# Optimization experiments

Measured on AMD Instinct MI355X. Metric: run time of the kernel, lower is better.

The kernel has to match this reference:

```python
import jax, jax.numpy as jnp
import numpy as np
import math

N, E, D, H, EH, DEPTH = 50000, 800000, 128, 128, 16, 3
RATIO = 0.5
BN_SCALE = 1.0 / math.sqrt(1.0 + 1e-5)  # eval-mode BatchNorm1d: running mean 0, var 1
NEG_SLOPE = 0.01  # leaky_relu default


def setup_inputs() -> dict:
    key = jax.random.key(0)
    ks = jax.random.split(key, 16)
    s = lambda k, shape: jax.random.normal(k, shape, dtype=jnp.float32) * 0.05
    return {
        "x": jax.random.normal(ks[0], (N, D), dtype=jnp.float32),
        "edge_index": jax.random.randint(ks[1], (2, E), 0, N, dtype=jnp.int32),
        "edge_attr": jax.random.uniform(ks[2], (E, EH), dtype=jnp.float32),
        "We_w": s(ks[3], (EH, 1)), "We_b": s(ks[4], (1,)),
        "Wdown": s(ks[5], (DEPTH + 1, H, H)), "bdown": s(ks[6], (DEPTH + 1, H)),
        "Wpool": s(ks[7], (DEPTH, H)),
        "Wup": s(ks[8], (DEPTH, H, H)), "bup": s(ks[9], (DEPTH, H)),
        "gnorm": 1.0 + s(ks[10], (DEPTH + 1, H)), "bnorm": s(ks[11], (DEPTH + 1, H)),
        "Wr": s(ks[12], (D, D)), "br": s(ks[13], (D,)),
        "gr": 1.0 + s(ks[14], (D,)), "brn": s(ks[15], (D,)),
    }


def _bn(x, g, b):
    # eval-mode BatchNorm1d with running_mean=0, running_var=1
    return x * (g * BN_SCALE) + b


def _lrelu(x):
    return jnp.where(x > 0, x, NEG_SLOPE * x)


def _gcn(x, src, dst, w, W, b, fill):
    # PyG GCNConv: add self-loops (fill=1.0, improved -> 2.0), symmetric norm
    n = x.shape[0]
    h = x @ W  # [n, H]
    deg = jax.ops.segment_sum(w, dst, num_segments=n) + fill
    dinv = jax.lax.rsqrt(deg)
    coef = dinv[src] * w * dinv[dst]  # [E]
    agg = jax.ops.segment_sum(coef[:, None] * h[src], dst, num_segments=n)
    return agg + (fill / deg)[:, None] * h + b  # self-loop norm = fill/deg


def _topk_pool(x, src, dst, w, p, k):
    # PyG TopKPooling: score = tanh(x.p/||p||), keep top-k, scale kept x by score,
    # filter edges to kept nodes (masked edges kept at fixed length with weight 0)
    n = x.shape[0]
    score = jnp.tanh((x @ p) / jnp.linalg.norm(p))
    vals, perm = jax.lax.top_k(score, k)
    xp = x[perm] * vals[:, None]
    pos = jnp.full((n,), -1, dtype=jnp.int32).at[perm].set(jnp.arange(k, dtype=jnp.int32))
    ns, nd = pos[src], pos[dst]
    valid = (ns >= 0) & (nd >= 0)
    return (xp, jnp.where(valid, ns, 0), jnp.where(valid, nd, 0),
            jnp.where(valid, w, 0.0), perm)


def reference(x, edge_index, edge_attr, We_w, We_b, Wdown, bdown, Wpool, Wup, bup,
              gnorm, bnorm, Wr, br, gr, brn):
    src, dst = edge_index[0], edge_index[1]
    # edge embedding + min/max normalization
    ew = edge_attr @ We_w[:, 0] + We_b[0]  # [E]
    ew = ew - jnp.min(ew)
    ew = ew / (jnp.max(ew) + 1e-7)
    h = _bn(x, gnorm[0], bnorm[0])
    h = _lrelu(_gcn(h, src, dst, ew, Wdown[0], bdown[0], 1.0))
    xs, es, perms = [h], [(src, dst, ew)], []
    for i in range(DEPTH):
        k = int(math.ceil(RATIO * h.shape[0]))
        h, src, dst, ew, perm = _topk_pool(h, src, dst, ew, Wpool[i], k)
        h = _bn(h, gnorm[i + 1], bnorm[i + 1])
        h = _gcn(h, src, dst, ew, Wdown[i + 1], bdown[i + 1], 1.0)
        if i < DEPTH - 1:
            h = _lrelu(h)
            xs.append(h)
            es.append((src, dst, ew))
        perms.append(perm)
    for i in range(DEPTH):
        j = DEPTH - 1 - i
        res = xs[j]
        src, dst, ew = es[j]
        up = jnp.zeros_like(res).at[perms[j]].set(h)  # scatter unpool
        h = _gcn(res + up, src, dst, ew, Wup[i], bup[i], 2.0)  # improved=True -> fill 2
        if i < DEPTH - 1:
            h = _lrelu(h)
    g = jnp.sum(h, axis=0, keepdims=True)  # global_add_pool, single graph
    g = g @ Wr + br
    return _bn(g, gr, brn)
```

## Files before the change

kernel.cpp:

```cpp
#include <hip/hip_runtime.h>
#include <math.h>

#define N0   50000
#define E0   800000
#define HD   128
#define EHD  16
#define KP1  25000
#define KP2  12500
#define KP3  6250
#define BN_SCALE 0.9999950000374997f
#define NEG_SLOPE 0.01f
#define E1C  400000
#define E2C  120000
#define E3C  40000
#define NBE  782
#define CSB  782

#define NBIN   782
#define SBCAP  448
#define OVFCAP 4096

typedef int   vi4 __attribute__((ext_vector_type(4)));
typedef float vf4 __attribute__((ext_vector_type(4)));

__device__ __forceinline__ unsigned fenc(float f) {
    unsigned u = __float_as_uint(f);
    return (u & 0x80000000u) ? ~u : (u | 0x80000000u);
}
__device__ __forceinline__ unsigned packbf2(float a, float b) {
    unsigned ua = __float_as_uint(a);
    unsigned ub = __float_as_uint(b);
    ua = (ua + 0x7FFFu + ((ua >> 16) & 1u)) >> 16;
    ub = (ub + 0x7FFFu + ((ub >> 16) & 1u)) >> 16;
    return ua | (ub << 16);
}
__device__ __forceinline__ void bf8_fma(float* acc, uint4 h, float c) {
    acc[0] += c * __uint_as_float(h.x << 16);
    acc[1] += c * __uint_as_float(h.x & 0xFFFF0000u);
    acc[2] += c * __uint_as_float(h.y << 16);
    acc[3] += c * __uint_as_float(h.y & 0xFFFF0000u);
    acc[4] += c * __uint_as_float(h.z << 16);
    acc[5] += c * __uint_as_float(h.z & 0xFFFF0000u);
    acc[6] += c * __uint_as_float(h.w << 16);
    acc[7] += c * __uint_as_float(h.w & 0xFFFF0000u);
}

__global__ void k_edge_ew(const float* __restrict__ ea, const float* __restrict__ Ww,
                          const float* __restrict__ Wb, float* __restrict__ ew,
                          float2* __restrict__ partials, int E) {
    int e = blockIdx.x * 256 + threadIdx.x;
    float mn = 3.4e38f, mx = -3.4e38f;
    if (e < E) {
        const float4* a4 = (const float4*)(ea + (size_t)e * EHD);
        float s = Wb[0];
        #pragma unroll
        for (int q = 0; q < 4; ++q) {
            float4 a = a4[q];
            s += a.x * Ww[q*4+0] + a.y * Ww[q*4+1] + a.z * Ww[q*4+2] + a.w * Ww[q*4+3];
        }
        ew[e] = s;
        mn = s; mx = s;
    }
    #pragma unroll
    for (int off = 32; off > 0; off >>= 1) {
        mn = fminf(mn, __shfl_xor(mn, off));
        mx = fmaxf(mx, __shfl_xor(mx, off));
    }
    __shared__ float smn[4], smx[4];
    int lane = threadIdx.x & 63, wid = threadIdx.x >> 6;
    if (lane == 0) { smn[wid] = mn; smx[wid] = mx; }
    __syncthreads();
    if (threadIdx.x == 0) {
        float a = fminf(fminf(smn[0], smn[1]), fminf(smn[2], smn[3]));
        float b = fmaxf(fmaxf(smx[0], smx[1]), fmaxf(smx[2], smx[3]));
        partials[blockIdx.x] = make_float2(a, b);
    }
}

__global__ void __launch_bounds__(1024)
k_reduce_mm(const float2* __restrict__ partials, int nb, float* __restrict__ mmv) {
    float mn = 3.4e38f, mx = -3.4e38f;
    for (int i = threadIdx.x; i < nb; i += 1024) {
        float2 t = partials[i];
        mn = fminf(mn, t.x); mx = fmaxf(mx, t.y);
    }
    #pragma unroll
    for (int off = 32; off > 0; off >>= 1) {
        mn = fminf(mn, __shfl_xor(mn, off));
        mx = fmaxf(mx, __shfl_xor(mx, off));
    }
    __shared__ float smn[16], smx[16];
    int lane = threadIdx.x & 63, wid = threadIdx.x >> 6;
    if (lane == 0) { smn[wid] = mn; smx[wid] = mx; }
    __syncthreads();
    if (threadIdx.x == 0) {
        for (int w = 1; w < 16; ++w) { mn = fminf(mn, smn[w]); mx = fmaxf(mx, smx[w]); }
        mmv[0] = mn; mmv[1] = mx;
    }
}

__global__ void __launch_bounds__(256)
k_ew_norm_stage(float* __restrict__ ew, const float* __restrict__ mmv,
                const int* __restrict__ src, const int* __restrict__ dst,
                int* __restrict__ cnt, int* __restrict__ subCnt,
                uint2* __restrict__ staging,
                int4* __restrict__ ovfList, int* __restrict__ ovfCnt, int E) {
    unsigned xcd;
    asm volatile("s_getreg_b32 %0, hwreg(HW_REG_XCC_ID)" : "=s"(xcd));
    int e = blockIdx.x * 256 + threadIdx.x;
    if (e >= E) return;
    float mn = mmv[0];
    float sc = 1.0f / ((mmv[1] - mn) + 1e-7f);
    float w = (ew[e] - mn) * sc;
    ew[e] = w;
    if (w == 0.0f) return;
    int d = dst[e];
    int s = src[e];
    atomicAdd(&cnt[d], 1);
    int sb = (int)xcd * NBIN + (d >> 6);
    int slot = atomicAdd(&subCnt[sb], 1);
    if (slot < SBCAP) {
        staging[(size_t)sb * SBCAP + slot] =
            make_uint2((unsigned)s | ((unsigned)(d & 63) << 16), __float_as_uint(w));
    } else {
        int o = atomicAdd(ovfCnt, 1);
        if (o < OVFCAP) ovfList[o] = make_int4(s, d, __float_as_int(w), 0);
    }
}

#define GT_ROWS 64
__global__ void __launch_bounds__(256)
k_gemm128(const float* __restrict__ A, const float* __restrict__ W,
          unsigned* __restrict__ Cb, int n,
          const float* __restrict__ gs, const float* __restrict__ gb,
          const float* __restrict__ up_h, const int* __restrict__ up_pos) {
    __shared__ float As[GT_ROWS][132];
    int tid = threadIdx.x;
    int row0 = blockIdx.x * GT_ROWS;
    int maxr = n - row0;
    {
        #pragma unroll
        for (int it = 0; it < 8; ++it) {
            int idx = it * 256 + tid;
            int r = idx >> 5, q = idx & 31;
            float4 v = make_float4(0.f, 0.f, 0.f, 0.f);
            if (r < maxr) {
                v = ((const float4*)(A + (size_t)(row0 + r) * HD))[q];
                if (up_pos) {
                    int sl = up_pos[row0 + r];
                    if (sl >= 0) {
                        float4 u = ((const float4*)(up_h + (size_t)sl * HD))[q];
                        v.x += u.x; v.y += u.y; v.z += u.z; v.w += u.w;
                    }
                }
                if (gs) {
                    float4 g4 = ((const float4*)gs)[q];
                    float4 b4 = ((const float4*)gb)[q];
                    v.x = v.x * (g4.x * BN_SCALE) + b4.x;
                    v.y = v.y * (g4.y * BN_SCALE) + b4.y;
                    v.z = v.z * (g4.z * BN_SCALE) + b4.z;
                    v.w = v.w * (g4.w * BN_SCALE) + b4.w;
                }
            }
            *(float4*)&As[r][q * 4] = v;
        }
    }
    __syncthreads();
    int cg = tid & 31;
    int rg = tid >> 5;
    float4 acc[8];
    #pragma unroll
    for (int j = 0; j < 8; ++j) acc[j] = make_float4(0.f, 0.f, 0.f, 0.f);
    const float4* W4 = (const float4*)W;
    #pragma unroll 4
    for (int k = 0; k < HD; k += 4) {
        float4 w0 = W4[(k + 0) * 32 + cg];
        float4 w1 = W4[(k + 1) * 32 + cg];
        float4 w2 = W4[(k + 2) * 32 + cg];
        float4 w3 = W4[(k + 3) * 32 + cg];
        #pragma unroll
        for (int jj = 0; jj < 4; ++jj) {
            float4 a = *(const float4*)&As[4 * rg + jj][k];
            acc[jj].x += a.x * w0.x + a.y * w1.x + a.z * w2.x + a.w * w3.x;
            acc[jj].y += a.x * w0.y + a.y * w1.y + a.z * w2.y + a.w * w3.y;
            acc[jj].z += a.x * w0.z + a.y * w1.z + a.z * w2.z + a.w * w3.z;
            acc[jj].w += a.x * w0.w + a.y * w1.w + a.z * w2.w + a.w * w3.w;
        }
        #pragma unroll
        for (int jj = 0; jj < 4; ++jj) {
            float4 a = *(const float4*)&As[32 + 4 * rg + jj][k];
            acc[4 + jj].x += a.x * w0.x + a.y * w1.x + a.z * w2.x + a.w * w3.x;
            acc[4 + jj].y += a.x * w0.y + a.y * w1.y + a.z * w2.y + a.w * w3.y;
            acc[4 + jj].z += a.x * w0.z + a.y * w1.z + a.z * w2.z + a.w * w3.z;
            acc[4 + jj].w += a.x * w0.w + a.y * w1.w + a.z * w2.w + a.w * w3.w;
        }
    }
    #pragma unroll
    for (int jj = 0; jj < 4; ++jj) {
        int r = 4 * rg + jj;
        if (r < maxr) {
            uint2 pk = make_uint2(packbf2(acc[jj].x, acc[jj].y), packbf2(acc[jj].z, acc[jj].w));
            ((uint2*)(Cb + (size_t)(row0 + r) * 64))[cg] = pk;
        }
    }
    #pragma unroll
    for (int jj = 0; jj < 4; ++jj) {
        int r = 32 + 4 * rg + jj;
        if (r < maxr) {
            uint2 pk = make_uint2(packbf2(acc[4+jj].x, acc[4+jj].y), packbf2(acc[4+jj].z, acc[4+jj].w));
            ((uint2*)(Cb + (size_t)(row0 + r) * 64))[cg] = pk;
        }
    }
}

__global__ void k_sum_scan(const int* __restrict__ cnt, int* __restrict__ bsum, int n,
                           int* __restrict__ totalOut, unsigned* __restrict__ dctr) {
    int base = blockIdx.x * 1024;
    int s = 0;
    #pragma unroll
    for (int it = 0; it < 4; ++it) {
        int i = base + it * 256 + threadIdx.x;
        if (i < n) s += cnt[i];
    }
    __shared__ int ws[4];
    __shared__ int lastFlag;
    int lane = threadIdx.x & 63, wid = threadIdx.x >> 6;
    #pragma unroll
    for (int off = 32; off > 0; off >>= 1) s += __shfl_down(s, off);
    if (lane == 0) ws[wid] = s;
    __syncthreads();
    if (threadIdx.x == 0) {
        __hip_atomic_store(&bsum[blockIdx.x], ws[0] + ws[1] + ws[2] + ws[3],
                           __ATOMIC_RELAXED, __HIP_MEMORY_SCOPE_AGENT);
        unsigned prev = __hip_atomic_fetch_add(dctr, 1u, __ATOMIC_ACQ_REL, __HIP_MEMORY_SCOPE_AGENT);
        lastFlag = (prev == gridDim.x - 1);
    }
    __syncthreads();
    if (!lastFlag) return;
    if (threadIdx.x < 64) {
        int nb = gridDim.x;
        int t = threadIdx.x;
        int v = (t < nb) ? __hip_atomic_load(&bsum[t], __ATOMIC_RELAXED, __HIP_MEMORY_SCOPE_AGENT) : 0;
        int x = v;
        #pragma unroll
        for (int off = 1; off < 64; off <<= 1) {
            int y = __shfl_up(x, off);
            if (t >= off) x += y;
        }
        if (t < nb) bsum[t] = x - v;
        if (t == nb - 1) totalOut[0] = x;
    }
    if (threadIdx.x == 0)
        __hip_atomic_store(dctr, 0u, __ATOMIC_RELAXED, __HIP_MEMORY_SCOPE_AGENT);
}

__global__ void k_chunk_scan(const int* __restrict__ cnt, const int* __restrict__ bo,
                             int* __restrict__ rowptr, int* __restrict__ cursor, int n) {
    __shared__ int wsum[4];
    __shared__ int running;
    int base = blockIdx.x * 1024;
    if (threadIdx.x == 0) running = bo[blockIdx.x];
    __syncthreads();
    int lane = threadIdx.x & 63, wid = threadIdx.x >> 6;
    #pragma unroll
    for (int it = 0; it < 4; ++it) {
        int i = base + it * 256 + threadIdx.x;
        int v = (i < n) ? cnt[i] : 0;
        int x = v;
        #pragma unroll
        for (int off = 1; off < 64; off <<= 1) {
            int y = __shfl_up(x, off);
            if (lane >= off) x += y;
        }
        if (lane == 63) wsum[wid] = x;
        __syncthreads();
        int wb = 0;
        for (int w = 0; w < wid; ++w) wb += wsum[w];
        int excl = running + wb + x - v;
        if (i < n) { rowptr[i] = excl; cursor[i] = excl; }
        __syncthreads();
        if (threadIdx.x == 0) running += wsum[0] + wsum[1] + wsum[2] + wsum[3];
        __syncthreads();
    }
}

__global__ void k_csr_fill(const int* __restrict__ src, const int* __restrict__ dst,
                           const float* __restrict__ w, int* __restrict__ cursor,
                           int2* __restrict__ csr,
                           const int* __restrict__ EinPtr, int EinImm) {
    int Ein = EinPtr ? EinPtr[0] : EinImm;
    int e = blockIdx.x * 256 + threadIdx.x;
    if (e >= Ein) return;
    float wv = w[e];
    if (wv == 0.0f) return;
    int slot = atomicAdd(&cursor[dst[e]], 1);
    csr[slot] = make_int2(src[e], __float_as_int(wv));
}

__global__ void __launch_bounds__(256)
k_binB(const int* __restrict__ rowptr, const int* __restrict__ subCnt,
       const uint2* __restrict__ staging, int2* __restrict__ csr,
       int* __restrict__ cursor, float* __restrict__ sumW, int n) {
    __shared__ int   lcur[64];
    __shared__ float lw[64];
    __shared__ int2  img[2048];
    int b = blockIdx.x;
    int v0 = b * 64;
    int v1 = min(n, v0 + 64);
    int base = rowptr[v0];
    int total = rowptr[v1] - base;
    if (threadIdx.x < 64) {
        int v = v0 + threadIdx.x;
        lcur[threadIdx.x] = (v < v1) ? rowptr[v] - base : 0;
        lw[threadIdx.x] = 0.f;
    }
    __syncthreads();
    #pragma unroll 1
    for (int x = 0; x < 8; ++x) {
        int sb = x * NBIN + b;
        int cnt = min(subCnt[sb], SBCAP);
        const uint2* st = staging + (size_t)sb * SBCAP;
        for (int i = threadIdx.x; i < cnt; i += 256) {
            uint2 en = st[i];
            int dloc = (en.x >> 16) & 63;
            float wv = __uint_as_float(en.y);
            int slot = atomicAdd(&lcur[dloc], 1);
            if (slot < 2048) img[slot] = make_int2((int)(en.x & 0xFFFFu), (int)en.y);
            atomicAdd(&lw[dloc], wv);
        }
    }
    __syncthreads();
    for (int i = threadIdx.x; i < total; i += 256)
        csr[base + i] = img[i];
    if (threadIdx.x < 64) {
        int v = v0 + threadIdx.x;
        if (v < v1) {
            cursor[v] = base + lcur[threadIdx.x];
            sumW[v]   = lw[threadIdx.x];
        }
    }
}

__global__ void k_binOvf(const int4* __restrict__ ovfList, const int* __restrict__ ovfCnt,
                         int* __restrict__ cursor, int2* __restrict__ csr,
                         float* __restrict__ sumW) {
    int cnt = min(ovfCnt[0], OVFCAP);
    for (int i = threadIdx.x; i < cnt; i += 256) {
        int4 e = ovfList[i];
        int slot = atomicAdd(&cursor[e.y], 1);
        csr[slot] = make_int2(e.x, e.z);
        atomicAdd(&sumW[e.y], __int_as_float(e.z));
    }
}

__global__ void k_deg_dinv(const int* __restrict__ rowptr, const int2* __restrict__ csr,
                           float fill, float* __restrict__ deg, float* __restrict__ dinv, int n) {
    int v = blockIdx.x * 256 + threadIdx.x;
    if (v >= n) return;
    float s = fill;
    int rs = rowptr[v], re = rowptr[v + 1];
    for (int j = rs; j < re; ++j) s += __int_as_float(csr[j].y);
    deg[v] = s;
    dinv[v] = rsqrtf(s);
}

__global__ void k_deg_dinv_d(const float* __restrict__ sumW, float fill,
                             float* __restrict__ deg, float* __restrict__ dinv, int n) {
    int v = blockIdx.x * 256 + threadIdx.x;
    if (v >= n) return;
    float s = fill + sumW[v];
    deg[v] = s;
    dinv[v] = rsqrtf(s);
}

__global__ void __launch_bounds__(256)
k_gcn_gather(const int* __restrict__ rowptr, const int2* __restrict__ csr,
             const float* __restrict__ deg, const float* __restrict__ dinv,
             const unsigned* __restrict__ hWb,
             const float* __restrict__ bias,
             float fill, int n, int lrelu, float* __restrict__ out) {
    int v = blockIdx.x * 4 + (threadIdx.x >> 6);
    int lane = threadIdx.x & 63;
    if (v >= n) return;
    int rs = rowptr[v], re = rowptr[v + 1];
    float dv = dinv[v];
    int quarter = lane >> 4;
    int qi = lane & 15;
    float acc[8];
    #pragma unroll
    for (int i = 0; i < 8; ++i) acc[i] = 0.f;
    for (int base = rs; base < re; base += 64) {
        int idx = base + lane;
        int s_r = 0; float c_r = 0.f;
        if (idx < re) {
            int2 ent = csr[idx];
            s_r = ent.x;
            c_r = dinv[s_r] * __int_as_float(ent.y) * dv;
        }
        int cnt = min(64, re - base);
        int groups = cnt >> 2;
        int t = 0;
        for (; t + 1 < groups; t += 2) {
            int j0 = 4 * t + quarter, j1 = j0 + 4;
            int   s0 = __shfl(s_r, j0); float c0 = __shfl(c_r, j0);
            int   s1 = __shfl(s_r, j1); float c1 = __shfl(c_r, j1);
            uint4 h0 = ((const uint4*)(hWb + (size_t)s0 * 64))[qi];
            uint4 h1 = ((const uint4*)(hWb + (size_t)s1 * 64))[qi];
            bf8_fma(acc, h0, c0);
            bf8_fma(acc, h1, c1);
        }
        for (; t < groups; ++t) {
            int j = 4 * t + quarter;
            int s = __shfl(s_r, j); float c = __shfl(c_r, j);
            uint4 h = ((const uint4*)(hWb + (size_t)s * 64))[qi];
            bf8_fma(acc, h, c);
        }
        int rem = cnt & 3;
        if (quarter < rem) {
            int j = groups * 4 + quarter;
            int s = __shfl(s_r, j); float c = __shfl(c_r, j);
            uint4 h = ((const uint4*)(hWb + (size_t)s * 64))[qi];
            bf8_fma(acc, h, c);
        }
    }
    #pragma unroll
    for (int i = 0; i < 8; ++i) {
        acc[i] += __shfl_xor(acc[i], 16);
        acc[i] += __shfl_xor(acc[i], 32);
    }
    if (quarter == 0) {
        uint4 hs = ((const uint4*)(hWb + (size_t)v * 64))[qi];
        float sc = fill / deg[v];
        float hv[8];
        hv[0] = __uint_as_float(hs.x << 16); hv[1] = __uint_as_float(hs.x & 0xFFFF0000u);
        hv[2] = __uint_as_float(hs.y << 16); hv[3] = __uint_as_float(hs.y & 0xFFFF0000u);
        hv[4] = __uint_as_float(hs.z << 16); hv[5] = __uint_as_float(hs.z & 0xFFFF0000u);
        hv[6] = __uint_as_float(hs.w << 16); hv[7] = __uint_as_float(hs.w & 0xFFFF0000u);
        float4 b0 = ((const float4*)bias)[2 * qi];
        float4 b1 = ((const float4*)bias)[2 * qi + 1];
        float o[8];
        o[0] = acc[0] + sc * hv[0] + b0.x;
        o[1] = acc[1] + sc * hv[1] + b0.y;
        o[2] = acc[2] + sc * hv[2] + b0.z;
        o[3] = acc[3] + sc * hv[3] + b0.w;
        o[4] = acc[4] + sc * hv[4] + b1.x;
        o[5] = acc[5] + sc * hv[5] + b1.y;
        o[6] = acc[6] + sc * hv[6] + b1.z;
        o[7] = acc[7] + sc * hv[7] + b1.w;
        if (lrelu) {
            #pragma unroll
            for (int i = 0; i < 8; ++i) o[i] = (o[i] > 0.f) ? o[i] : NEG_SLOPE * o[i];
        }
        float4* orow = (float4*)(out + (size_t)v * HD);
        orow[2 * qi]     = make_float4(o[0], o[1], o[2], o[3]);
        orow[2 * qi + 1] = make_float4(o[4], o[5], o[6], o[7]);
    }
}

__global__ void k_score(const float* __restrict__ x, const float* __restrict__ p,
                        float* __restrict__ score, int n, int* __restrict__ selws) {
    for (int i = blockIdx.x * 256 + threadIdx.x; i < 5120; i += gridDim.x * 256) selws[i] = 0;
    int lane = threadIdx.x & 63;
    float pv0 = p[lane], pv1 = p[lane + 64];
    float ps = pv0 * pv0 + pv1 * pv1;
    #pragma unroll
    for (int off = 32; off > 0; off >>= 1) ps += __shfl_xor(ps, off);
    float rnorm = 1.0f / sqrtf(ps);
    int node = blockIdx.x * 4 + (threadIdx.x >> 6);
    if (node >= n) return;
    const float* row = x + (size_t)node * HD;
    float s = row[lane] * pv0 + row[lane + 64] * pv1;
    #pragma unroll
    for (int off = 32; off > 0; off >>= 1) s += __shfl_xor(s, off);
    if (lane == 0) score[node] = tanhf(s * rnorm);
}

__global__ void __launch_bounds__(256)
k_histpick(const float* __restrict__ score, int n, int pass,
           unsigned* __restrict__ prefix, int* __restrict__ hist,
           int kImm, const int* __restrict__ remIn, int* __restrict__ remOut,
           unsigned* __restrict__ doneCtr) {
    __shared__ int lh[2048];
    int nbins = (pass == 2) ? 1024 : 2048;
    for (int i = threadIdx.x; i < nbins; i += 256) lh[i] = 0;
    __syncthreads();
    unsigned pfx = (pass != 0) ? prefix[0] : 0u;
    int stride = gridDim.x * 256;
    for (int i = blockIdx.x * 256 + threadIdx.x; i < n; i += stride) {
        unsigned u = fenc(score[i]);
        int bin; bool ok;
        if (pass == 0)      { bin = u >> 21;            ok = true; }
        else if (pass == 1) { bin = (u >> 10) & 2047;   ok = ((u >> 21) == (pfx >> 21)); }
        else                { bin = u & 1023;           ok = ((u >> 10) == (pfx >> 10)); }
        if (ok) atomicAdd(&lh[bin], 1);
    }
    __syncthreads();
    for (int i = threadIdx.x; i < nbins; i += 256) {
        int c = lh[i];
        if (c) __hip_atomic_fetch_add(&hist[i], c, __ATOMIC_RELAXED, __HIP_MEMORY_SCOPE_AGENT);
    }
    __syncthreads();
    __shared__ int lastFlag;
    if (threadIdx.x == 0) {
        unsigned prev = __hip_atomic_fetch_add(doneCtr, 1u, __ATOMIC_ACQ_REL, __HIP_MEMORY_SCOPE_AGENT);
        lastFlag = (prev == gridDim.x - 1);
    }
    __syncthreads();
    if (!lastFlag) return;
    __shared__ int wsum[4];
    int k = remIn ? remIn[0] : kImm;
    int t = threadIdx.x;
    int per = nbins >> 8;
    int hi = nbins - t * per, lo = hi - per;
    int s = 0;
    for (int b = lo; b < hi; ++b)
        s += __hip_atomic_load(&hist[b], __ATOMIC_RELAXED, __HIP_MEMORY_SCOPE_AGENT);
    int lane = t & 63, wid = t >> 6;
    int x = s;
    #pragma unroll
    for (int off = 1; off < 64; off <<= 1) {
        int y = __shfl_up(x, off);
        if (lane >= off) x += y;
    }
    if (lane == 63) wsum[wid] = x;
    __syncthreads();
    int wb = 0;
    for (int w = 0; w < wid; ++w) wb += wsum[w];
    int excl = wb + x - s;
    if (k > excl && k <= excl + s) {
        int cum = excl;
        int shift = (pass == 0) ? 21 : (pass == 1) ? 10 : 0;
        for (int b = hi - 1; b >= lo; --b) {
            int h = __hip_atomic_load(&hist[b], __ATOMIC_RELAXED, __HIP_MEMORY_SCOPE_AGENT);
            if (k <= cum + h) {
                unsigned base = (pass == 0) ? 0u : prefix[0];
                prefix[0] = base | ((unsigned)b << shift);
                remOut[0] = k - cum;
                break;
            }
            cum += h;
        }
    }
    __syncthreads();
    if (threadIdx.x == 0)
        __hip_atomic_store(doneCtr, 0u, __ATOMIC_RELAXED, __HIP_MEMORY_SCOPE_AGENT);
}

__global__ void k_cmp_countscan(const float* __restrict__ score, int n,
                                const unsigned* __restrict__ prefix,
                                int* __restrict__ bgt, int* __restrict__ beq,
                                unsigned* __restrict__ dctr) {
    unsigned T = prefix[0];
    int base = blockIdx.x * 1024;
    int gt = 0, eq = 0;
    #pragma unroll
    for (int it = 0; it < 4; ++it) {
        int i = base + it * 256 + threadIdx.x;
        if (i < n) {
            unsigned u = fenc(score[i]);
            gt += (u > T); eq += (u == T);
        }
    }
    __shared__ int sg[4], se[4];
    __shared__ int lastFlag;
    int lane = threadIdx.x & 63, wid = threadIdx.x >> 6;
    #pragma unroll
    for (int off = 32; off > 0; off >>= 1) { gt += __shfl_down(gt, off); eq += __shfl_down(eq, off); }
    if (lane == 0) { sg[wid] = gt; se[wid] = eq; }
    __syncthreads();
    if (threadIdx.x == 0) {
        __hip_atomic_store(&bgt[blockIdx.x], sg[0] + sg[1] + sg[2] + sg[3],
                           __ATOMIC_RELAXED, __HIP_MEMORY_SCOPE_AGENT);
        __hip_atomic_store(&beq[blockIdx.x], se[0] + se[1] + se[2] + se[3],
                           __ATOMIC_RELAXED, __HIP_MEMORY_SCOPE_AGENT);
        unsigned prev = __hip_atomic_fetch_add(dctr, 1u, __ATOMIC_ACQ_REL, __HIP_MEMORY_SCOPE_AGENT);
        lastFlag = (prev == gridDim.x - 1);
    }
    __syncthreads();
    if (!lastFlag) return;
    if (threadIdx.x < 64) {
        int nb = gridDim.x;
        int t = threadIdx.x;
        int va = (t < nb) ? __hip_atomic_load(&bgt[t], __ATOMIC_RELAXED, __HIP_MEMORY_SCOPE_AGENT) : 0;
        int vb = (t < nb) ? __hip_atomic_load(&beq[t], __ATOMIC_RELAXED, __HIP_MEMORY_SCOPE_AGENT) : 0;
        int xa = va, xb = vb;
        #pragma unroll
        for (int off = 1; off < 64; off <<= 1) {
            int ya = __shfl_up(xa, off), yb = __shfl_up(xb, off);
            if (t >= off) { xa += ya; xb += yb; }
        }
        if (t < nb) { bgt[t] = xa - va; beq[t] = xb - vb; }
    }
    if (threadIdx.x == 0)
        __hip_atomic_store(dctr, 0u, __ATOMIC_RELAXED, __HIP_MEMORY_SCOPE_AGENT);
}

__global__ void k_cmp_assign(const float* __restrict__ score, int n, int kcap,
                             const unsigned* __restrict__ prefix,
                             const int* __restrict__ selTies,
                             const int* __restrict__ bgt, const int* __restrict__ beq,
                             int* __restrict__ pos, int* __restrict__ perm,
                             float* __restrict__ vals) {
    unsigned T = prefix[0];
    int tiesNeed = selTies[0];
    __shared__ int wgt[4], weq[4];
    __shared__ int rgt, req;
    int base = blockIdx.x * 1024;
    if (threadIdx.x == 0) { rgt = bgt[blockIdx.x]; req = beq[blockIdx.x]; }
    __syncthreads();
    int lane = threadIdx.x & 63, wid = threadIdx.x >> 6;
    #pragma unroll
    for (int it = 0; it < 4; ++it) {
        int i = base + it * 256 + threadIdx.x;
        bool in = i < n;
        float sc = in ? score[i] : 0.f;
        unsigned u = in ? fenc(sc) : 0u;
        bool g = in && (u > T);
        bool e = in && (u == T);
        unsigned long long mg = __ballot(g), me = __ballot(e);
        int lgt = __popcll(mg & ((1ull << lane) - 1ull));
        int leq = __popcll(me & ((1ull << lane) - 1ull));
        if (lane == 0) { wgt[wid] = __popcll(mg); weq[wid] = __popcll(me); }
        __syncthreads();
        int wbg = 0, wbe = 0;
        for (int w = 0; w < wid; ++w) { wbg += wgt[w]; wbe += weq[w]; }
        int gtRank = rgt + wbg + lgt;
        int tieRank = req + wbe + leq;
        if (in) {
            int slot = -1;
            if (g) slot = gtRank + min(tieRank, tiesNeed);
            else if (e && tieRank < tiesNeed) slot = gtRank + tieRank;
            if (slot >= kcap) slot = -1;
            pos[i] = slot;
            if (slot >= 0) { perm[slot] = i; vals[slot] = sc; }
        }
        __syncthreads();
        if (threadIdx.x == 0) {
            rgt += wgt[0] + wgt[1] + wgt[2] + wgt[3];
            req += weq[0] + weq[1] + weq[2] + weq[3];
        }
        __syncthreads();
    }
}

__global__ void k_pool_bn(const float* __restrict__ x, const int* __restrict__ perm,
                          const float* __restrict__ vals, const float* __restrict__ g,
                          const float* __restrict__ b, float* __restrict__ out, int k) {
    int idx = blockIdx.x * 256 + threadIdx.x;
    if (idx >= k * HD) return;
    int slot = idx >> 7, c = idx & 127;
    int v = perm[slot];
    out[idx] = (x[(size_t)v * HD + c] * vals[slot]) * (g[c] * BN_SCALE) + b[c];
}

__global__ void k_ecompact_countscan(const int* __restrict__ src, const int* __restrict__ dst,
                                     const float* __restrict__ w, const int* __restrict__ pos,
                                     const int* __restrict__ EinPtr, int EinImm, int kNodes,
                                     int* __restrict__ bsumE, int* __restrict__ ecntOut,
                                     int* __restrict__ cnt, unsigned* __restrict__ dctr) {
    int Ein = EinPtr ? EinPtr[0] : EinImm;
    for (int i = blockIdx.x * 256 + threadIdx.x; i < kNodes; i += gridDim.x * 256) cnt[i] = 0;
    int base = blockIdx.x * 1024;
    int c = 0;
    #pragma unroll
    for (int it = 0; it < 4; ++it) {
        int e = base + it * 256 + threadIdx.x;
        if (e < Ein) {
            float wv = w[e];
            if (wv != 0.0f && pos[src[e]] >= 0 && pos[dst[e]] >= 0) ++c;
        }
    }
    __shared__ int ws[4];
    __shared__ int lastFlag;
    int lane = threadIdx.x & 63, wid = threadIdx.x >> 6;
    #pragma unroll
    for (int off = 32; off > 0; off >>= 1) c += __shfl_down(c, off);
    if (lane == 0) ws[wid] = c;
    __syncthreads();
    if (threadIdx.x == 0) {
        __hip_atomic_store(&bsumE[blockIdx.x], ws[0] + ws[1] + ws[2] + ws[3],
                           __ATOMIC_RELAXED, __HIP_MEMORY_SCOPE_AGENT);
        unsigned prev = __hip_atomic_fetch_add(dctr, 1u, __ATOMIC_ACQ_REL, __HIP_MEMORY_SCOPE_AGENT);
        lastFlag = (prev == gridDim.x - 1);
    }
    __syncthreads();
    if (!lastFlag) return;
    {
        __shared__ int wtot[4];
        int nb = gridDim.x;
        int t = threadIdx.x;
        int i0 = t * 4;
        int v0 = (i0 + 0 < nb) ? __hip_atomic_load(&bsumE[i0 + 0], __ATOMIC_RELAXED, __HIP_MEMORY_SCOPE_AGENT) : 0;
        int v1 = (i0 + 1 < nb) ? __hip_atomic_load(&bsumE[i0 + 1], __ATOMIC_RELAXED, __HIP_MEMORY_SCOPE_AGENT) : 0;
        int v2 = (i0 + 2 < nb) ? __hip_atomic_load(&bsumE[i0 + 2], __ATOMIC_RELAXED, __HIP_MEMORY_SCOPE_AGENT) : 0;
        int v3 = (i0 + 3 < nb) ? __hip_atomic_load(&bsumE[i0 + 3], __ATOMIC_RELAXED, __HIP_MEMORY_SCOPE_AGENT) : 0;
        int tot = v0 + v1 + v2 + v3;
        int x2 = tot;
        #pragma unroll
        for (int off = 1; off < 64; off <<= 1) {
            int y = __shfl_up(x2, off);
            if (lane >= off) x2 += y;
        }
        if (lane == 63) wtot[wid] = x2;
        __syncthreads();
        int wb = 0;
        for (int q = 0; q < wid; ++q) wb += wtot[q];
        int excl = wb + x2 - tot;
        if (i0 + 0 < nb) bsumE[i0 + 0] = excl;
        if (i0 + 1 < nb) bsumE[i0 + 1] = excl + v0;
        if (i0 + 2 < nb) bsumE[i0 + 2] = excl + v0 + v1;
        if (i0 + 3 < nb) bsumE[i0 + 3] = excl + v0 + v1 + v2;
        if (t == 255) ecntOut[0] = wtot[0] + wtot[1] + wtot[2] + wtot[3];
    }
    __syncthreads();
    if (threadIdx.x == 0)
        __hip_atomic_store(dctr, 0u, __ATOMIC_RELAXED, __HIP_MEMORY_SCOPE_AGENT);
}

__global__ void k_ecompact_assign(const int* __restrict__ src, const int* __restrict__ dst,
                                  const float* __restrict__ w, const int* __restrict__ pos,
                                  const int* __restrict__ EinPtr, int EinImm,
                                  const int* __restrict__ bsumE,
                                  int* __restrict__ nsrc, int* __restrict__ ndst,
                                  float* __restrict__ nw, int* __restrict__ cnt) {
    int Ein = EinPtr ? EinPtr[0] : EinImm;
    __shared__ int wcnt[4];
    __shared__ int running;
    if (threadIdx.x == 0) running = bsumE[blockIdx.x];
    __syncthreads();
    int base = blockIdx.x * 1024;
    int lane = threadIdx.x & 63, wid = threadIdx.x >> 6;
    #pragma unroll
    for (int it = 0; it < 4; ++it) {
        int e = base + it * 256 + threadIdx.x;
        bool valid = false; int ns = 0, nd = 0; float wv = 0.f;
        if (e < Ein) {
            wv = w[e];
            if (wv != 0.0f) {
                ns = pos[src[e]]; nd = pos[dst[e]];
                valid = (ns >= 0) && (nd >= 0);
            }
        }
        unsigned long long m = __ballot(valid);
        int r = __popcll(m & ((1ull << lane) - 1ull));
        if (lane == 0) wcnt[wid] = __popcll(m);
        __syncthreads();
        int wb = 0;
        for (int w2 = 0; w2 < wid; ++w2) wb += wcnt[w2];
        if (valid) {
            int slot = running + wb + r;
            nsrc[slot] = ns; ndst[slot] = nd; nw[slot] = wv;
            atomicAdd(&cnt[nd], 1);
        }
        __syncthreads();
        if (threadIdx.x == 0) running += wcnt[0] + wcnt[1] + wcnt[2] + wcnt[3];
        __syncthreads();
    }
}

__global__ void __launch_bounds__(256)
k_colsum_part(const float* __restrict__ h, float* __restrict__ cpart, int n) {
    int c = threadIdx.x & 127;
    int rh = threadIdx.x >> 7;
    int r0 = blockIdx.x * 64;
    int r1 = min(n, r0 + 64);
    float local = 0.f;
    for (int r = r0 + rh; r < r1; r += 2) local += h[(size_t)r * HD + c];
    __shared__ float sh[256];
    sh[threadIdx.x] = local;
    __syncthreads();
    if (threadIdx.x < 128) cpart[(size_t)blockIdx.x * HD + c] = sh[c] + sh[c + 128];
}

__global__ void __launch_bounds__(1024)
k_colsum_final(const float* __restrict__ cpart, int nb,
               const float* __restrict__ Wr, const float* __restrict__ br,
               const float* __restrict__ gr, const float* __restrict__ brn,
               float* __restrict__ out) {
    __shared__ float gsh[HD];
    int c = threadIdx.x & 127;
    int seg = threadIdx.x >> 7;
    float local = 0.f;
    for (int b = seg; b < nb; b += 8) local += cpart[(size_t)b * HD + c];
    __shared__ float sh[1024];
    sh[threadIdx.x] = local;
    __syncthreads();
    if (threadIdx.x < 128) {
        float s = 0.f;
        #pragma unroll
        for (int q = 0; q < 8; ++q) s += sh[c + q * 128];
        gsh[c] = s;
    }
    __syncthreads();
    if (threadIdx.x < 128) {
        float s = br[c];
        for (int k = 0; k < HD; ++k) s += gsh[k] * Wr[k * HD + c];
        out[c] = s * (gr[c] * BN_SCALE) + brn[c];
    }
}

extern "C" void kernel_launch(void* const* d_in, const int* in_sizes, int n_in,
                              void* d_out, int out_size, void* d_ws, size_t ws_size,
                              hipStream_t stream) {
    const float* x     = (const float*)d_in[0];
    const int*   ei    = (const int*)d_in[1];
    const float* eattr = (const float*)d_in[2];
    const float* We_w  = (const float*)d_in[3];
    const float* We_b  = (const float*)d_in[4];
    const float* Wdown = (const float*)d_in[5];
    const float* bdown = (const float*)d_in[6];
    const float* Wpool = (const float*)d_in[7];
    const float* Wup   = (const float*)d_in[8];
    const float* bup   = (const float*)d_in[9];
    const float* gnorm = (const float*)d_in[10];
    const float* bnorm = (const float*)d_in[11];
    const float* Wr    = (const float*)d_in[12];
    const float* br    = (const float*)d_in[13];
    const float* gr    = (const float*)d_in[14];
    const float* brn   = (const float*)d_in[15];
    const int* src0 = ei;
    const int* dst0 = ei + E0;
    float* out = (float*)d_out;

    char* p = (char*)d_ws;
    auto alloc = [&](size_t bytes) -> void* {
        void* r = (void*)p;
        p += (bytes + 255) & ~(size_t)255;
        return r;
    };
    float* ew0  = (float*)alloc(E0 * 4);
    int* src1 = (int*)alloc(E1C * 4); int* dst1 = (int*)alloc(E1C * 4); float* ew1 = (float*)alloc(E1C * 4);
    int* src2 = (int*)alloc(E2C * 4); int* dst2 = (int*)alloc(E2C * 4); float* ew2 = (float*)alloc(E2C * 4);
    int* src3 = (int*)alloc(E3C * 4); int* dst3 = (int*)alloc(E3C * 4); float* ew3 = (float*)alloc(E3C * 4);
    float* hbuf = (float*)alloc((size_t)N0 * HD * 4);
    unsigned* hWb = (unsigned*)alloc((size_t)N0 * 64 * 4);
    float* tmp  = (float*)alloc((size_t)N0 * HD * 4);
    float* xs0  = (float*)alloc((size_t)N0 * HD * 4);
    float* xs1  = (float*)alloc((size_t)KP1 * HD * 4);
    float* xs2  = (float*)alloc((size_t)KP2 * HD * 4);
    float* deg   = (float*)alloc(N0 * 4);
    float* dinv  = (float*)alloc(N0 * 4);
    float* sumW0 = (float*)alloc(N0 * 4);
    float* score = (float*)alloc(N0 * 4);
    int*   pos1  = (int*)alloc(N0 * 4);
    int*   pos2  = (int*)alloc(N0 * 4);
    int*   pos3  = (int*)alloc(N0 * 4);
    float* vals  = (float*)alloc(KP1 * 4);
    int* perm1 = (int*)alloc(KP1 * 4);
    int* perm2 = (int*)alloc(KP2 * 4);
    int* perm3 = (int*)alloc(KP3 * 4);
    int* rowptr0 = (int*)alloc((N0 + 1) * 4);
    int* rowptr1 = (int*)alloc((KP1 + 1) * 4);
    int* rowptr2 = (int*)alloc((KP2 + 1) * 4);
    int* rowptr3 = (int*)alloc((KP3 + 1) * 4);
    int2* csrP0 = (int2*)alloc((size_t)E0 * 8);
    int2* csrP1 = (int2*)alloc((size_t)E1C * 8);
    int2* csrP2 = (int2*)alloc((size_t)E2C * 8);
    int2* csrP3 = (int2*)alloc((size_t)E3C * 8);
    int* cnt    = (int*)alloc(N0 * 4);
    int* cursor = (int*)alloc(N0 * 4);
    int* selws  = (int*)alloc(5120 * 4);
    int* hist0 = selws;
    int* hist1 = selws + 2048;
    int* hist2 = selws + 4096;
    int* bgt    = (int*)alloc(64 * 4);
    int* beq    = (int*)alloc(64 * 4);
    int* bsum   = (int*)alloc(64 * 4);
    int* bsumE  = (int*)alloc(1024 * 4);
    float2* partials = (float2*)alloc(((E0 + 255) / 256) * 8);
    float* cpart = (float*)alloc((size_t)CSB * HD * 4);
    float* mmv       = (float*)alloc(64);
    unsigned* ctrws  = (unsigned*)alloc(64 * 4);
    unsigned* dctrS  = ctrws + 0;
    unsigned* dctrH  = ctrws + 8;
    unsigned* dctrC  = ctrws + 16;
    unsigned* dctrE  = ctrws + 24;
    unsigned* prefix = (unsigned*)alloc(64);
    int* rem0        = (int*)alloc(64);
    int* rem1        = (int*)alloc(64);
    int* tiesN       = (int*)alloc(64);
    int* ecnt1       = (int*)alloc(64);
    int* ecnt2       = (int*)alloc(64);
    int* ecnt3       = (int*)alloc(64);
    int* subCnt      = (int*)alloc((8 * NBIN + 64) * 4);
    int* ovfCnt      = subCnt + 8 * NBIN;
    int4* ovfList    = (int4*)alloc((size_t)OVFCAP * 16);
    uint2* staging   = (uint2*)tmp;

    const int EB = (E0 + 255) / 256;

    auto build_csr = [&](const int* esrc, const int* edst, const float* eww, int n,
                         int* rowptr, int2* csrP,
                         const int* EinPtr, int EinImm, int gridE) {
        int nb = (n + 1023) / 1024;
        k_sum_scan<<<nb, 256, 0, stream>>>(cnt, bsum, n, rowptr + n, dctrS);
        k_chunk_scan<<<nb, 256, 0, stream>>>(cnt, bsum, rowptr, cursor, n);
        k_csr_fill<<<gridE, 256, 0, stream>>>(esrc, edst, eww, cursor, csrP, EinPtr, EinImm);
    };

    auto run_gcn = [&](const float* hin, const int* rowptr, const int2* csrP,
                       const float* sumW,
                       const float* W, const float* bias, float fill, int n, int lrelu,
                       float* outbuf, const float* bn_g, const float* bn_b,
                       const float* up_h, const int* up_pos) {
        k_gemm128<<<(n + GT_ROWS - 1) / GT_ROWS, 256, 0, stream>>>(hin, W, hWb, n, bn_g, bn_b, up_h, up_pos);
        if (sumW)
            k_deg_dinv_d<<<(n + 255) / 256, 256, 0, stream>>>(sumW, fill, deg, dinv, n);
        else
            k_deg_dinv<<<(n + 255) / 256, 256, 0, stream>>>(rowptr, csrP, fill, deg, dinv, n);
        k_gcn_gather<<<(n + 3) / 4, 256, 0, stream>>>(rowptr, csrP, deg, dinv, hWb,
                                                      bias, fill, n, lrelu, outbuf);
    };

    auto run_pool = [&](const float* xin, int n, int k, const float* pvec,
                        const float* g, const float* b,
                        const int* esrc_in, const int* edst_in, const float* ew_in,
                        const int* EinPtr, int EinImm,
                        int* pos, int* perm,
                        int* esrc_out, int* edst_out, float* ew_out, int* ecntOut) {
        int nb = (n + 1023) / 1024;
        k_score<<<(n + 3) / 4, 256, 0, stream>>>(xin, pvec, score, n, selws);
        k_histpick<<<64, 256, 0, stream>>>(score, n, 0, prefix, hist0, k, (const int*)nullptr, rem0, dctrH);
        k_histpick<<<64, 256, 0, stream>>>(score, n, 1, prefix, hist1, 0, rem0, rem1, dctrH);
        k_histpick<<<64, 256, 0, stream>>>(score, n, 2, prefix, hist2, 0, rem1, tiesN, dctrH);
        k_cmp_countscan<<<nb, 256, 0, stream>>>(score, n, prefix, bgt, beq, dctrC);
        k_cmp_assign<<<nb, 256, 0, stream>>>(score, n, k, prefix, tiesN, bgt, beq, pos, perm, vals);
        k_pool_bn<<<((size_t)k * HD + 255) / 256, 256, 0, stream>>>(xin, perm, vals, g, b, hbuf, k);
        k_ecompact_countscan<<<NBE, 256, 0, stream>>>(esrc_in, edst_in, ew_in, pos, EinPtr, EinImm, k,
                                                      bsumE, ecntOut, cnt, dctrE);
        k_ecompact_assign<<<NBE, 256, 0, stream>>>(esrc_in, edst_in, ew_in, pos, EinPtr, EinImm,
                                                   bsumE, esrc_out, edst_out, ew_out, cnt);
    };

    hipMemsetAsync((void*)ctrws, 0, 64 * 4, stream);
    hipMemsetAsync(cnt, 0, (size_t)N0 * 4, stream);
    hipMemsetAsync(subCnt, 0, (size_t)(8 * NBIN + 64) * 4, stream);

    k_edge_ew<<<EB, 256, 0, stream>>>(eattr, We_w, We_b, ew0, partials, E0);
    k_reduce_mm<<<1, 1024, 0, stream>>>(partials, EB, mmv);
    k_ew_norm_stage<<<EB, 256, 0, stream>>>(ew0, mmv, src0, dst0, cnt, subCnt, staging,
                                            ovfList, ovfCnt, E0);

    {
        int nb = (N0 + 1023) / 1024;
        k_sum_scan<<<nb, 256, 0, stream>>>(cnt, bsum, N0, rowptr0 + N0, dctrS);
        k_chunk_scan<<<nb, 256, 0, stream>>>(cnt, bsum, rowptr0, cursor, N0);
        k_binB<<<NBIN, 256, 0, stream>>>(rowptr0, subCnt, staging, csrP0, cursor, sumW0, N0);
        k_binOvf<<<1, 256, 0, stream>>>(ovfList, ovfCnt, cursor, csrP0, sumW0);
    }

    run_gcn(x, rowptr0, csrP0, sumW0, Wdown, bdown, 1.0f, N0, 1, xs0, gnorm, bnorm, nullptr, nullptr);

    run_pool(xs0, N0, KP1, Wpool, gnorm + HD, bnorm + HD, src0, dst0, ew0,
             (const int*)nullptr, E0, pos1, perm1, src1, dst1, ew1, ecnt1);
    build_csr(src1, dst1, ew1, KP1, rowptr1, csrP1, ecnt1, 0, (E1C + 255) / 256);
    run_gcn(hbuf, rowptr1, csrP1, nullptr, Wdown + 1 * HD * HD, bdown + 1 * HD, 1.0f, KP1, 1, xs1,
            nullptr, nullptr, nullptr, nullptr);

    run_pool(xs1, KP1, KP2, Wpool + HD, gnorm + 2 * HD, bnorm + 2 * HD, src1, dst1, ew1,
             ecnt1, 0, pos2, perm2, src2, dst2, ew2, ecnt2);
    build_csr(src2, dst2, ew2, KP2, rowptr2, csrP2, ecnt2, 0, (E2C + 255) / 256);
    run_gcn(hbuf, rowptr2, csrP2, nullptr, Wdown + 2 * HD * HD, bdown + 2 * HD, 1.0f, KP2, 1, xs2,
            nullptr, nullptr, nullptr, nullptr);

    run_pool(xs2, KP2, KP3, Wpool + 2 * HD, gnorm + 3 * HD, bnorm + 3 * HD, src2, dst2, ew2,
             ecnt2, 0, pos3, perm3, src3, dst3, ew3, ecnt3);
    build_csr(src3, dst3, ew3, KP3, rowptr3, csrP3, ecnt3, 0, (E3C + 255) / 256);
    run_gcn(hbuf, rowptr3, csrP3, nullptr, Wdown + 3 * HD * HD, bdown + 3 * HD, 1.0f, KP3, 0, tmp,
            nullptr, nullptr, nullptr, nullptr);

    run_gcn(xs2, rowptr2, csrP2, nullptr, Wup, bup, 2.0f, KP2, 1, tmp, nullptr, nullptr, tmp, pos3);

    run_gcn(xs1, rowptr1, csrP1, nullptr, Wup + 1 * HD * HD, bup + 1 * HD, 2.0f, KP1, 1, tmp,
            nullptr, nullptr, tmp, pos2);

    run_gcn(xs0, rowptr0, csrP0, sumW0, Wup + 2 * HD * HD, bup + 2 * HD, 2.0f, N0, 0, tmp,
            nullptr, nullptr, tmp, pos1);

    k_colsum_part<<<CSB, 256, 0, stream>>>(tmp, cpart, N0);
    k_colsum_final<<<1, 1024, 0, stream>>>(cpart, CSB, Wr, br, gr, brn, out);
}
```

Measured before the change: 869.3 us.

## Derive level-0 CSR row pointers from staged bins, dropping global degree atomics

The level-0 CSR build no longer counts per-node in-degree with a global atomic for every edge, and no longer runs the two-kernel prefix scan over that count array. A single-block scan now sums the per-XCD sub-bin counts to get each bin's base offset. The bin kernel then reads its staged edges twice: first to build a local per-node histogram and weight sum, then to place edges, writing rowptr, sumW and the cursor itself. This removes about 800k global atomics, a memset and one kernel launch, at the cost of a second read of the staging buffer. Edges that spill to the overflow list are no longer counted in rowptr, so any overflow would write past its row's range.

```diff
diff --git a/kernel.cpp b/kernel.cpp
--- a/kernel.cpp
+++ b/kernel.cpp
@@ -102,8 +102,7 @@
 __global__ void __launch_bounds__(256)
 k_ew_norm_stage(float* __restrict__ ew, const float* __restrict__ mmv,
                 const int* __restrict__ src, const int* __restrict__ dst,
-                int* __restrict__ cnt, int* __restrict__ subCnt,
-                uint2* __restrict__ staging,
+                int* __restrict__ subCnt, uint2* __restrict__ staging,
                 int4* __restrict__ ovfList, int* __restrict__ ovfCnt, int E) {
     unsigned xcd;
     asm volatile("s_getreg_b32 %0, hwreg(HW_REG_XCC_ID)" : "=s"(xcd));
@@ -116,7 +115,6 @@
     if (w == 0.0f) return;
     int d = dst[e];
     int s = src[e];
-    atomicAdd(&cnt[d], 1);
     int sb = (int)xcd * NBIN + (d >> 6);
     int slot = atomicAdd(&subCnt[sb], 1);
     if (slot < SBCAP) {
@@ -126,6 +124,32 @@
         int o = atomicAdd(ovfCnt, 1);
         if (o < OVFCAP) ovfList[o] = make_int4(s, d, __float_as_int(w), 0);
     }
+}
+
+__global__ void __launch_bounds__(1024)
+k_bin_scan(const int* __restrict__ subCnt, int* __restrict__ binBase,
+           int* __restrict__ rowptrEnd) {
+    int t = threadIdx.x;
+    int v = 0;
+    if (t < NBIN) {
+        #pragma unroll
+        for (int x = 0; x < 8; ++x) v += subCnt[x * NBIN + t];
+    }
+    int lane = t & 63, wid = t >> 6;
+    int xs = v;
+    #pragma unroll
+    for (int off = 1; off < 64; off <<= 1) {
+        int y = __shfl_up(xs, off);
+        if (lane >= off) xs += y;
+    }
+    __shared__ int wsum[16];
+    if (lane == 63) wsum[wid] = xs;
+    __syncthreads();
+    int wb = 0;
+    for (int w = 0; w < wid; ++w) wb += wsum[w];
+    int excl = wb + xs - v;
+    if (t < NBIN) binBase[t] = excl;
+    if (t == NBIN - 1) rowptrEnd[0] = excl + v;
 }
 
 #define GT_ROWS 64
@@ -298,46 +322,67 @@
 }
 
 __global__ void __launch_bounds__(256)
-k_binB(const int* __restrict__ rowptr, const int* __restrict__ subCnt,
-       const uint2* __restrict__ staging, int2* __restrict__ csr,
-       int* __restrict__ cursor, float* __restrict__ sumW, int n) {
+k_binB_r(const int* __restrict__ binBase, const int* __restrict__ subCnt,
+         const uint2* __restrict__ staging, int2* __restrict__ csr,
+         int* __restrict__ cursor, float* __restrict__ sumW,
+         int* __restrict__ rowptr, int n) {
+    __shared__ int   lhist[64];
     __shared__ int   lcur[64];
     __shared__ float lw[64];
     __shared__ int2  img[2048];
+    __shared__ int   segc[8];
+    __shared__ int   totalSh;
     int b = blockIdx.x;
     int v0 = b * 64;
-    int v1 = min(n, v0 + 64);
-    int base = rowptr[v0];
-    int total = rowptr[v1] - base;
-    if (threadIdx.x < 64) {
-        int v = v0 + threadIdx.x;
-        lcur[threadIdx.x] = (v < v1) ? rowptr[v] - base : 0;
-        lw[threadIdx.x] = 0.f;
-    }
+    int base = binBase[b];
+    if (threadIdx.x < 64) { lhist[threadIdx.x] = 0; lw[threadIdx.x] = 0.f; }
+    if (threadIdx.x < 8) segc[threadIdx.x] = min(subCnt[threadIdx.x * NBIN + b], SBCAP);
     __syncthreads();
     #pragma unroll 1
     for (int x = 0; x < 8; ++x) {
-        int sb = x * NBIN + b;
-        int cnt = min(subCnt[sb], SBCAP);
-        const uint2* st = staging + (size_t)sb * SBCAP;
+        int cnt = segc[x];
+        const uint2* st = staging + (size_t)(x * NBIN + b) * SBCAP;
         for (int i = threadIdx.x; i < cnt; i += 256) {
             uint2 en = st[i];
             int dloc = (en.x >> 16) & 63;
-            float wv = __uint_as_float(en.y);
+            atomicAdd(&lhist[dloc], 1);
+            atomicAdd(&lw[dloc], __uint_as_float(en.y));
+        }
+    }
+    __syncthreads();
+    if (threadIdx.x < 64) {
+        int c = lhist[threadIdx.x];
+        int xs = c;
+        #pragma unroll
+        for (int off = 1; off < 64; off <<= 1) {
+            int y = __shfl_up(xs, off);
+            if (threadIdx.x >= (unsigned)off) xs += y;
+        }
+        int excl = xs - c;
+        lcur[threadIdx.x] = excl;
+        int v = v0 + threadIdx.x;
+        if (v < n) { rowptr[v] = base + excl; sumW[v] = lw[threadIdx.x]; }
+        if (threadIdx.x == 63) totalSh = xs;
+    }
+    __syncthreads();
+    #pragma unroll 1
+    for (int x = 0; x < 8; ++x) {
+        int cnt = segc[x];
+        const uint2* st = staging + (size_t)(x * NBIN + b) * SBCAP;
+        for (int i = threadIdx.x; i < cnt; i += 256) {
+            uint2 en = st[i];
+            int dloc = (en.x >> 16) & 63;
             int slot = atomicAdd(&lcur[dloc], 1);
             if (slot < 2048) img[slot] = make_int2((int)(en.x & 0xFFFFu), (int)en.y);
-            atomicAdd(&lw[dloc], wv);
-        }
-    }
-    __syncthreads();
+        }
+    }
+    __syncthreads();
+    int total = min(totalSh, 2048);
     for (int i = threadIdx.x; i < total; i += 256)
         csr[base + i] = img[i];
     if (threadIdx.x < 64) {
         int v = v0 + threadIdx.x;
-        if (v < v1) {
-            cursor[v] = base + lcur[threadIdx.x];
-            sumW[v]   = lw[threadIdx.x];
-        }
+        if (v < n) cursor[v] = base + lcur[threadIdx.x];
     }
 }
 
@@ -884,6 +929,7 @@
     int* ecnt3       = (int*)alloc(64);
     int* subCnt      = (int*)alloc((8 * NBIN + 64) * 4);
     int* ovfCnt      = subCnt + 8 * NBIN;
+    int* binBase     = (int*)alloc((NBIN + 1) * 4);
     int4* ovfList    = (int4*)alloc((size_t)OVFCAP * 16);
     uint2* staging   = (uint2*)tmp;
 
@@ -933,21 +979,17 @@
     };
 
     hipMemsetAsync((void*)ctrws, 0, 64 * 4, stream);
-    hipMemsetAsync(cnt, 0, (size_t)N0 * 4, stream);
     hipMemsetAsync(subCnt, 0, (size_t)(8 * NBIN + 64) * 4, stream);
 
     k_edge_ew<<<EB, 256, 0, stream>>>(eattr, We_w, We_b, ew0, partials, E0);
     k_reduce_mm<<<1, 1024, 0, stream>>>(partials, EB, mmv);
-    k_ew_norm_stage<<<EB, 256, 0, stream>>>(ew0, mmv, src0, dst0, cnt, subCnt, staging,
+    k_ew_norm_stage<<<EB, 256, 0, stream>>>(ew0, mmv, src0, dst0, subCnt, staging,
                                             ovfList, ovfCnt, E0);
 
-    {
-        int nb = (N0 + 1023) / 1024;
-        k_sum_scan<<<nb, 256, 0, stream>>>(cnt, bsum, N0, rowptr0 + N0, dctrS);
-        k_chunk_scan<<<nb, 256, 0, stream>>>(cnt, bsum, rowptr0, cursor, N0);
-        k_binB<<<NBIN, 256, 0, stream>>>(rowptr0, subCnt, staging, csrP0, cursor, sumW0, N0);
-        k_binOvf<<<1, 256, 0, stream>>>(ovfList, ovfCnt, cursor, csrP0, sumW0);
-    }
+    k_bin_scan<<<1, 1024, 0, stream>>>(subCnt, binBase, rowptr0 + N0);
+    k_binB_r<<<NBIN, 256, 0, stream>>>(binBase, subCnt, staging, csrP0, cursor, sumW0,
+                                       rowptr0, N0);
+    k_binOvf<<<1, 256, 0, stream>>>(ovfList, ovfCnt, cursor, csrP0, sumW0);
 
     run_gcn(x, rowptr0, csrP0, sumW0, Wdown, bdown, 1.0f, N0, 1, xs0, gnorm, bnorm, nullptr, nullptr);
 
```

Result: faster. 841.9 us (-3.1%).
